# Kernel tuning notes

Hardware: AMD Instinct MI355X
Metric: run time of the kernel (lower is better)

## Reference

```python
import jax, jax.numpy as jnp
import numpy as np

NUM_USERS = 100000
NUM_ITEMS = 50000
EMB_DIM = 64
NUM_LAYERS = 3
NUM_EDGES = 1000000


def _xavier(key, shape):
    fan_in, fan_out = shape[-1], shape[-2] if len(shape) > 1 else shape[-1]
    limit = float(np.sqrt(6.0 / (fan_in + fan_out)))
    return jax.random.uniform(key, shape, jnp.float32, -limit, limit)


def setup_inputs() -> dict:
    key = jax.random.key(0)
    ks = jax.random.split(key, 8)
    edge_u = jax.random.randint(ks[0], (NUM_EDGES,), 0, NUM_USERS)
    edge_i = jax.random.randint(ks[1], (NUM_EDGES,), 0, NUM_ITEMS)
    u_emb = _xavier(ks[2], (NUM_USERS, EMB_DIM))
    i_emb = _xavier(ks[3], (NUM_ITEMS, EMB_DIM))
    Wgc = _xavier(ks[4], (NUM_LAYERS, EMB_DIM, EMB_DIM))
    Wbi = _xavier(ks[5], (NUM_LAYERS, EMB_DIM, EMB_DIM))
    bgc = jnp.zeros((NUM_LAYERS, EMB_DIM), jnp.float32)
    bbi = jnp.zeros((NUM_LAYERS, EMB_DIM), jnp.float32)
    return {"u_emb": u_emb, "i_emb": i_emb, "Wgc": Wgc, "bgc": bgc,
            "Wbi": Wbi, "bbi": bbi, "edge_u": edge_u, "edge_i": edge_i}


def _smooth(X, src, dst, dv_isqrt, de_inv, num_v, num_e):
    # HGNN smoothing: D_v^{-1/2} H D_e^{-1} H^T D_v^{-1/2} X via edge list
    X1 = X * dv_isqrt[:, None]
    E = jax.ops.segment_sum(X1[src], dst, num_segments=num_e) * de_inv[:, None]
    Y = jax.ops.segment_sum(E[dst], src, num_segments=num_v)
    return Y * dv_isqrt[:, None]


def reference(u_emb, i_emb, Wgc, bgc, Wbi, bbi, edge_u, edge_i):
    NU, NI, D = u_emb.shape[0], i_emb.shape[0], u_emb.shape[1]
    ones = jnp.ones((edge_u.shape[0],), jnp.float32)
    deg_u = jax.ops.segment_sum(ones, edge_u, num_segments=NU)
    deg_i = jax.ops.segment_sum(ones, edge_i, num_segments=NI)
    du_isqrt = jnp.where(deg_u > 0, deg_u, 1.0) ** -0.5 * (deg_u > 0)
    di_isqrt = jnp.where(deg_i > 0, deg_i, 1.0) ** -0.5 * (deg_i > 0)
    du_inv = jnp.where(deg_u > 0, 1.0 / jnp.where(deg_u > 0, deg_u, 1.0), 0.0)
    di_inv = jnp.where(deg_i > 0, 1.0 / jnp.where(deg_i > 0, deg_i, 1.0), 0.0)

    all_embs = jnp.concatenate([u_emb, i_emb], axis=0)
    embs_list = [all_embs]
    for l in range(Wgc.shape[0]):
        u, i = all_embs[:NU], all_embs[NU:]
        # hg_ui: users = vertices, items = hyperedges
        u_s = _smooth(u, edge_u, edge_i, du_isqrt, di_inv, NU, NI)
        # hg_iu: items = vertices, users = hyperedges
        i_s = _smooth(i, edge_i, edge_u, di_isqrt, du_inv, NI, NU)
        g = jnp.concatenate([u_s, i_s], axis=0)
        sum_embs = jax.nn.leaky_relu(g @ Wgc[l].T + bgc[l] + all_embs, negative_slope=0.2)
        bi_embs = jax.nn.leaky_relu((all_embs * g) @ Wbi[l].T + bbi[l], negative_slope=0.2)
        all_embs = sum_embs + bi_embs  # dropout off (eval mode)
        norm = jnp.sqrt(jnp.sum(all_embs * all_embs, axis=1, keepdims=True))
        all_embs = all_embs / jnp.maximum(norm, 1e-12)
        embs_list.append(all_embs)
    embs = jnp.mean(jnp.stack(embs_list, axis=1), axis=1)
    return embs[:NU], embs[NU:]
```

## Files before the change

### kernel.cpp

```cpp
#include <hip/hip_runtime.h>
#include <cstdint>
#include <cstddef>

#define NU 100000
#define NI 50000
#define NTOT 150000
#define EDIM 64
#define NE 1000000
#define NLAYERS 3
#define NTILES (NTOT / 16)
#define NPAIR (NTOT / 2)

#define NBKT 256
#define NPB 586
#define BCAP 13312
#define BCUR_STRIDE 16
#define BIN_EPB 1024
#define BIN_NBLK ((NE + BIN_EPB - 1) / BIN_EPB)
#define LCAP 28
#define LPAD 29
#define SLICE_CAP 13312

typedef __attribute__((ext_vector_type(8))) short short8;
typedef __attribute__((ext_vector_type(4))) float floatx4;

__device__ inline unsigned short f2bf(float f) {
    unsigned u = __float_as_uint(f);
    u += 0x7fffu + ((u >> 16) & 1u);
    return (unsigned short)(u >> 16);
}
__device__ inline unsigned pack_bf2(float a, float b) {
    unsigned ua = __float_as_uint(a); ua += 0x7fffu + ((ua >> 16) & 1u);
    unsigned ub = __float_as_uint(b); ub += 0x7fffu + ((ub >> 16) & 1u);
    return (ua >> 16) | (ub & 0xffff0000u);
}
__device__ inline float bf_lo(unsigned u) { return __uint_as_float(u << 16); }
__device__ inline float bf_hi(unsigned u) { return __uint_as_float(u & 0xffff0000u); }

__global__ __launch_bounds__(256) void k_binpairs(const int* __restrict__ eu,
                                                  const int* __restrict__ ei,
                                                  unsigned* __restrict__ bcur,
                                                  unsigned* __restrict__ bbuf) {
    __shared__ unsigned lbuf[NBKT * LPAD];
    __shared__ int lcnt[NBKT];
    int t = threadIdx.x;
    if (t < NBKT) lcnt[t] = 0;
    __syncthreads();
    int ebase = blockIdx.x * BIN_EPB + t;
#pragma unroll
    for (int k = 0; k < 4; ++k) {
        int e = ebase + k * 256;
        if (e < NE) {
            int u = eu[e];
            int v = NU + ei[e];
            int b0 = u / NPB;
            int w0 = ((u - b0 * NPB) << 18) | v;
            int p0 = atomicAdd(&lcnt[b0], 1);
            if (p0 < LCAP) lbuf[b0 * LPAD + p0] = (unsigned)w0;
            else {
                unsigned gp = atomicAdd(&bcur[b0 * BCUR_STRIDE], 1u);
                if (gp < BCAP) bbuf[(size_t)b0 * BCAP + gp] = (unsigned)w0;
            }
            int b1 = v / NPB;
            int w1 = ((v - b1 * NPB) << 18) | u;
            int p1 = atomicAdd(&lcnt[b1], 1);
            if (p1 < LCAP) lbuf[b1 * LPAD + p1] = (unsigned)w1;
            else {
                unsigned gp = atomicAdd(&bcur[b1 * BCUR_STRIDE], 1u);
                if (gp < BCAP) bbuf[(size_t)b1 * BCAP + gp] = (unsigned)w1;
            }
        }
    }
    __syncthreads();
    int nb = min(lcnt[t], LCAP);
    if (nb > 0) {
        unsigned gp = atomicAdd(&bcur[t * BCUR_STRIDE], (unsigned)nb);
        for (int i = 0; i < nb; ++i) {
            unsigned idx = gp + i;
            if (idx < BCAP) bbuf[(size_t)t * BCAP + idx] = lbuf[t * LPAD + i];
        }
    }
}

__global__ __launch_bounds__(1024) void k_buildcsr(
    const unsigned* __restrict__ bbuf, const unsigned* __restrict__ bcur,
    int* __restrict__ deg, int* __restrict__ start,
    float* __restrict__ isq, float* __restrict__ inv, int* __restrict__ csr,
    const float* __restrict__ ue, const float* __restrict__ ie,
    unsigned* __restrict__ snap0, unsigned* __restrict__ gbuf,
    unsigned* __restrict__ Ebuf,
    const float* __restrict__ Wg, const float* __restrict__ Wb,
    unsigned short* __restrict__ wgb, unsigned short* __restrict__ wbb) {
    __shared__ int slice[SLICE_CAP];
    __shared__ int lcur[NPB];
    __shared__ float sisq[NPB];
    __shared__ int bb_s, scnt_s;
    int b = blockIdx.x;
    int t = threadIdx.x;
    int n0 = b * NPB;
    int nn = NTOT - n0;
    if (nn > NPB) nn = NPB;
    if (nn < 0) nn = 0;
    if (t < NBKT) slice[t] = min((int)bcur[t * BCUR_STRIDE], BCAP);
    if (t < NPB) lcur[t] = 0;
    __syncthreads();
    for (int off = 1; off < NBKT; off <<= 1) {
        int tmp = (t < NBKT && t >= off) ? slice[t - off] : 0;
        __syncthreads();
        if (t < NBKT) slice[t] += tmp;
        __syncthreads();
    }
    if (t == 0) {
        int tb = min((int)bcur[b * BCUR_STRIDE], BCAP);
        scnt_s = tb;
        bb_s = slice[b] - tb;
    }
    __syncthreads();
    int c = scnt_s;
    int bb = bb_s;
    const unsigned* pb = bbuf + (size_t)b * BCAP;
    for (int i = t; i < c; i += 1024) atomicAdd(&lcur[(int)(pb[i] >> 18)], 1);
    __syncthreads();
    int cnt_t = (t < nn) ? lcur[t] : 0;
    slice[t] = cnt_t;
    __syncthreads();
    for (int off = 1; off < 1024; off <<= 1) {
        int tmp = (t >= off) ? slice[t - off] : 0;
        __syncthreads();
        slice[t] += tmp;
        __syncthreads();
    }
    int excl = slice[t] - cnt_t;
    int slen = slice[1023];
    if (t < nn) {
        int n = n0 + t;
        deg[n] = cnt_t;
        start[n] = bb + excl;
        float df = (float)cnt_t;
        float q = cnt_t > 0 ? 1.0f / sqrtf(df) : 0.f;
        isq[n] = q;
        sisq[t] = q;
        inv[n] = cnt_t > 0 ? 1.0f / df : 0.f;
    }
    __syncthreads();
    if (t < nn) lcur[t] = excl;
    __syncthreads();
    for (int i = t; i < c; i += 1024) {
        unsigned pr = pb[i];
        int idx = atomicAdd(&lcur[(int)(pr >> 18)], 1);
        if (idx < SLICE_CAP) slice[idx] = (int)(pr & 0x3FFFFu);
    }
    __syncthreads();
    if (slen > SLICE_CAP) slen = SLICE_CAP;
    for (int i = t; i < slen; i += 1024) csr[bb + i] = slice[i];
    for (int idx = t; idx < nn * 16; idx += 1024) {
        int r = idx >> 4, cc = idx & 15;
        int n = n0 + r;
        float4 v = (n < NU) ? ((const float4*)ue)[(size_t)n * 16 + cc]
                            : ((const float4*)ie)[(size_t)(n - NU) * 16 + cc];
        float s = sisq[r];
        uint2 bq, bs;
        bq.x = pack_bf2(v.x, v.y);
        bq.y = pack_bf2(v.z, v.w);
        bs.x = pack_bf2(v.x * s, v.y * s);
        bs.y = pack_bf2(v.z * s, v.w * s);
        ((uint2*)snap0)[(size_t)n * 16 + cc] = bq;
        ((uint2*)gbuf)[(size_t)n * 16 + cc] = bs;
    }
    if (b == 0) {
        for (int i = t; i < NLAYERS * 4096 / 4; i += 1024) {
            float4 g4 = ((const float4*)Wg)[i];
            float4 b4 = ((const float4*)Wb)[i];
            uint2 g, bq;
            g.x = pack_bf2(g4.x, g4.y); g.y = pack_bf2(g4.z, g4.w);
            bq.x = pack_bf2(b4.x, b4.y); bq.y = pack_bf2(b4.z, b4.w);
            ((uint2*)wgb)[i] = g;
            ((uint2*)wbb)[i] = bq;
        }
        if (t < 16) {
            ((uint2*)(Ebuf + NTOT * 32))[t] = make_uint2(0u, 0u);
            ((uint2*)(gbuf + NTOT * 32))[t] = make_uint2(0u, 0u);
        }
    }
}

__global__ __launch_bounds__(256) void k_gather(
    const unsigned* __restrict__ in_bf, unsigned* __restrict__ out_bf,
    const int* __restrict__ csr, const int* __restrict__ start,
    const int* __restrict__ deg, const float* __restrict__ sA) {
    int gw = (blockIdx.x * 256 + threadIdx.x) >> 6;
    int lane = threadIdx.x & 63;
    if (gw >= NPAIR) return;
    int l2 = lane & 31;
    int hbase = lane & 32;
    int row = gw * 2 + (lane >> 5);
    int s = l2 & 7;
    int g = l2 >> 3;
    int s0 = start[row];
    int dg = deg[row];
    float sc = sA[row];
    int dgo = __shfl_xor(dg, 32);
    int dgmax = max(dg, dgo);
    float aL0 = 0.f, aL1 = 0.f, aL2 = 0.f, aL3 = 0.f;
    float aH0 = 0.f, aH1 = 0.f, aH2 = 0.f, aH3 = 0.f;
    for (int j0 = 0; j0 < dgmax; j0 += 32) {
        int nidx = NTOT;
        if (j0 + l2 < dg) nidx = csr[s0 + j0 + l2];
        int jlim = min(32, dgmax - j0);
        for (int j = 0; j < jlim; j += 16) {
            int m0 = __shfl(nidx, hbase + j + g);
            int m1 = __shfl(nidx, hbase + j + 4 + g);
            int m2 = __shfl(nidx, hbase + j + 8 + g);
            int m3 = __shfl(nidx, hbase + j + 12 + g);
            uint4 u0 = *(const uint4*)(in_bf + (size_t)m0 * 32 + s * 4);
            uint4 u1 = *(const uint4*)(in_bf + (size_t)m1 * 32 + s * 4);
            uint4 u2 = *(const uint4*)(in_bf + (size_t)m2 * 32 + s * 4);
            uint4 u3 = *(const uint4*)(in_bf + (size_t)m3 * 32 + s * 4);
            aL0 += bf_lo(u0.x); aH0 += bf_hi(u0.x);
            aL1 += bf_lo(u0.y); aH1 += bf_hi(u0.y);
            aL2 += bf_lo(u0.z); aH2 += bf_hi(u0.z);
            aL3 += bf_lo(u0.w); aH3 += bf_hi(u0.w);
            aL0 += bf_lo(u1.x); aH0 += bf_hi(u1.x);
            aL1 += bf_lo(u1.y); aH1 += bf_hi(u1.y);
            aL2 += bf_lo(u1.z); aH2 += bf_hi(u1.z);
            aL3 += bf_lo(u1.w); aH3 += bf_hi(u1.w);
            aL0 += bf_lo(u2.x); aH0 += bf_hi(u2.x);
            aL1 += bf_lo(u2.y); aH1 += bf_hi(u2.y);
            aL2 += bf_lo(u2.z); aH2 += bf_hi(u2.z);
            aL3 += bf_lo(u2.w); aH3 += bf_hi(u2.w);
            aL0 += bf_lo(u3.x); aH0 += bf_hi(u3.x);
            aL1 += bf_lo(u3.y); aH1 += bf_hi(u3.y);
            aL2 += bf_lo(u3.z); aH2 += bf_hi(u3.z);
            aL3 += bf_lo(u3.w); aH3 += bf_hi(u3.w);
        }
    }
#pragma unroll
    for (int m = 8; m <= 16; m <<= 1) {
        aL0 += __shfl_xor(aL0, m); aH0 += __shfl_xor(aH0, m);
        aL1 += __shfl_xor(aL1, m); aH1 += __shfl_xor(aH1, m);
        aL2 += __shfl_xor(aL2, m); aH2 += __shfl_xor(aH2, m);
        aL3 += __shfl_xor(aL3, m); aH3 += __shfl_xor(aH3, m);
    }
    if (g == 0) {
        uint4 o;
        o.x = pack_bf2(sc * aL0, sc * aH0);
        o.y = pack_bf2(sc * aL1, sc * aH1);
        o.z = pack_bf2(sc * aL2, sc * aH2);
        o.w = pack_bf2(sc * aL3, sc * aH3);
        *(uint4*)(out_bf + (size_t)row * 32 + s * 4) = o;
    }
}

__global__ __launch_bounds__(256) void k_dense_mfma(
    const unsigned short* __restrict__ a_prev, unsigned* gbuf,
    unsigned short* __restrict__ snap_l, const float* __restrict__ isq,
    const unsigned short* __restrict__ wgb, const unsigned short* __restrict__ wbb,
    const float* __restrict__ bg, const float* __restrict__ bb, int writeScaled,
    int finalOut, const unsigned short* __restrict__ s1,
    const float* __restrict__ ue, const float* __restrict__ ie,
    float* __restrict__ outp) {
    int lane = threadIdx.x & 63;
    int lanelo = lane & 15;
    int quad = lane >> 4;
    int wid = (blockIdx.x * blockDim.x + threadIdx.x) >> 6;
    if (wid >= NTILES) return;

    short8 bWg[4][2], bWb[4][2];
#pragma unroll
    for (int t = 0; t < 4; ++t) {
#pragma unroll
        for (int h = 0; h < 2; ++h) {
            int n = t * 16 + lanelo;
            int k0 = h * 32 + quad * 8;
            bWg[t][h] = *(const short8*)&wgb[n * 64 + k0];
            bWb[t][h] = *(const short8*)&wbb[n * 64 + k0];
        }
    }
    float bgv[4], bbv[4];
#pragma unroll
    for (int t = 0; t < 4; ++t) {
        bgv[t] = bg[t * 16 + lanelo];
        bbv[t] = bb[t * 16 + lanelo];
    }

    int rbase = wid * 16;
    int arow = rbase + lanelo;
    short8 aG[2], aAG[2];
#pragma unroll
    for (int h = 0; h < 2; ++h) {
        uint4 ug = *(const uint4*)(gbuf + arow * 32 + h * 16 + quad * 4);
        uint4 ua = *(const uint4*)((const unsigned*)a_prev + arow * 32 + h * 16 + quad * 4);
        aG[h] = *(const short8*)&ug;
        uint4 up;
        up.x = pack_bf2(bf_lo(ua.x) * bf_lo(ug.x), bf_hi(ua.x) * bf_hi(ug.x));
        up.y = pack_bf2(bf_lo(ua.y) * bf_lo(ug.y), bf_hi(ua.y) * bf_hi(ug.y));
        up.z = pack_bf2(bf_lo(ua.z) * bf_lo(ug.z), bf_hi(ua.z) * bf_hi(ug.z));
        up.w = pack_bf2(bf_lo(ua.w) * bf_lo(ug.w), bf_hi(ua.w) * bf_hi(ug.w));
        aAG[h] = *(const short8*)&up;
    }
    floatx4 accg[4], accb[4];
#pragma unroll
    for (int t = 0; t < 4; ++t) {
        accg[t] = (floatx4)(0.f);
        accb[t] = (floatx4)(0.f);
    }
#pragma unroll
    for (int t = 0; t < 4; ++t) {
#pragma unroll
        for (int h = 0; h < 2; ++h) {
            accg[t] = __builtin_amdgcn_mfma_f32_16x16x32_bf16(aG[h], bWg[t][h], accg[t], 0, 0, 0);
            accb[t] = __builtin_amdgcn_mfma_f32_16x16x32_bf16(aAG[h], bWb[t][h], accb[t], 0, 0, 0);
        }
    }
    float nv[4][4];
    float ss[4] = {0.f, 0.f, 0.f, 0.f};
#pragma unroll
    for (int i = 0; i < 4; ++i) {
        int r = rbase + quad * 4 + i;
#pragma unroll
        for (int t = 0; t < 4; ++t) {
            float a = __uint_as_float((unsigned)a_prev[r * 64 + t * 16 + lanelo] << 16);
            float e1 = accg[t][i] + bgv[t] + a;
            e1 = e1 >= 0.f ? e1 : 0.2f * e1;
            float e2 = accb[t][i] + bbv[t];
            e2 = e2 >= 0.f ? e2 : 0.2f * e2;
            float v = e1 + e2;
            nv[i][t] = v;
            ss[i] += v * v;
        }
    }
#pragma unroll
    for (int m = 1; m < 16; m <<= 1) {
#pragma unroll
        for (int i = 0; i < 4; ++i) ss[i] += __shfl_xor(ss[i], m, 64);
    }
#pragma unroll
    for (int i = 0; i < 4; ++i) {
        int r = rbase + quad * 4 + i;
        float rn = 1.0f / fmaxf(sqrtf(ss[i]), 1e-12f);
        float sc = isq[r] * rn;
        if (finalOut) {
#pragma unroll
            for (int t = 0; t < 4; ++t) {
                int idx = r * 64 + t * 16 + lanelo;
                float rr = nv[i][t] * rn;
                float s1v = __uint_as_float((unsigned)s1[idx] << 16);
                float s2v = __uint_as_float((unsigned)a_prev[idx] << 16);
                float ev = (r < NU) ? ue[idx] : ie[idx - NU * 64];
                outp[idx] = 0.25f * (ev + s1v + s2v + rr);
            }
        } else {
#pragma unroll
            for (int t = 0; t < 4; ++t) {
                int idx = r * 64 + t * 16 + lanelo;
                float rr = nv[i][t] * rn;
                snap_l[idx] = f2bf(rr);
                if (writeScaled)
                    ((unsigned short*)gbuf)[idx] = f2bf(nv[i][t] * sc);
            }
        }
    }
}


extern "C" void kernel_launch(void* const* d_in, const int* in_sizes, int n_in,
                              void* d_out, int out_size, void* d_ws, size_t ws_size,
                              hipStream_t stream) {
    const float* u_emb = (const float*)d_in[0];
    const float* i_emb = (const float*)d_in[1];
    const float* Wgc = (const float*)d_in[2];
    const float* bgc = (const float*)d_in[3];
    const float* Wbi = (const float*)d_in[4];
    const float* bbi = (const float*)d_in[5];
    const int* edge_u = (const int*)d_in[6];
    const int* edge_i = (const int*)d_in[7];
    float* out = (float*)d_out;

    char* w = (char*)d_ws;
    auto alloc = [&](size_t bytes) {
        char* p = w;
        w += (bytes + 255) & ~(size_t)255;
        return p;
    };
    const size_t ROWBYTES = (size_t)(NTOT + 1) * EDIM * 2;
    int* deg = (int*)alloc((size_t)NTOT * 4);
    int* start = (int*)alloc((size_t)NTOT * 4);
    unsigned* bcur = (unsigned*)alloc((size_t)NBKT * BCUR_STRIDE * 4);
    int* csr = (int*)alloc((size_t)2 * NE * 4);
    float* isq = (float*)alloc((size_t)NTOT * 4);
    float* inv = (float*)alloc((size_t)NTOT * 4);
    unsigned short* wgb = (unsigned short*)alloc((size_t)NLAYERS * 4096 * 2);
    unsigned short* wbb = (unsigned short*)alloc((size_t)NLAYERS * 4096 * 2);
    unsigned* snap0 = (unsigned*)alloc((size_t)NTOT * EDIM * 2);
    unsigned* snap1 = (unsigned*)alloc((size_t)NTOT * EDIM * 2);
    unsigned* snap2 = (unsigned*)alloc((size_t)NTOT * EDIM * 2);
    unsigned* Ebuf = (unsigned*)alloc(ROWBYTES);
    unsigned* gbuf = (unsigned*)alloc(ROWBYTES);
    unsigned* bbuf = (unsigned*)snap1;

    hipMemsetAsync(bcur, 0, (size_t)NBKT * BCUR_STRIDE * 4, stream);
    k_binpairs<<<BIN_NBLK, 256, 0, stream>>>(edge_u, edge_i, bcur, bbuf);
    k_buildcsr<<<NBKT, 1024, 0, stream>>>(bbuf, bcur, deg, start, isq, inv, csr,
                                          u_emb, i_emb, snap0, gbuf, Ebuf,
                                          Wgc, Wbi, wgb, wbb);

    const int gatherBlocks = (NPAIR * 64 + 255) / 256;
    const int denseBlocks = (NTILES * 64 + 255) / 256;
    const unsigned short* aprev[3] = {(unsigned short*)snap0, (unsigned short*)snap1,
                                      (unsigned short*)snap2};
    unsigned short* snaps[3] = {(unsigned short*)snap1, (unsigned short*)snap2,
                                (unsigned short*)snap1 };
    for (int l = 0; l < NLAYERS; ++l) {
        k_gather<<<gatherBlocks, 256, 0, stream>>>(gbuf, Ebuf, csr, start, deg, inv);
        k_gather<<<gatherBlocks, 256, 0, stream>>>(Ebuf, gbuf, csr, start, deg, isq);
        k_dense_mfma<<<denseBlocks, 256, 0, stream>>>(
            aprev[l], gbuf, snaps[l], isq, wgb + (size_t)l * 4096, wbb + (size_t)l * 4096,
            bgc + (size_t)l * 64, bbi + (size_t)l * 64,
            l < NLAYERS - 1 ? 1 : 0,
            l == NLAYERS - 1 ? 1 : 0,
            (const unsigned short*)snap1, u_emb, i_emb, out);
    }
}
```

Measured before the change: 456.5 us.

## Pair gather rows by degree via per-block permutation and add 4-wide tail loop

While building the CSR, each block sorts its rows into a permutation by degree bucket (capped at 63), and the gather kernel processes rows in that order. Two rows that share a wavefront then have similar degrees, so less time is lost when one half waits on the other's longer neighbour list. The inner loop also gains a 4-neighbour remainder step, so leftover neighbours no longer run a full 16-wide iteration of padded loads. The cost is an extra perm array read per row and the loss of row-order locality in the gather output writes.

```diff
diff --git a/kernel.cpp b/kernel.cpp
--- a/kernel.cpp
+++ b/kernel.cpp
@@ -90,7 +90,8 @@
     unsigned* __restrict__ snap0, unsigned* __restrict__ gbuf,
     unsigned* __restrict__ Ebuf,
     const float* __restrict__ Wg, const float* __restrict__ Wb,
-    unsigned short* __restrict__ wgb, unsigned short* __restrict__ wbb) {
+    unsigned short* __restrict__ wgb, unsigned short* __restrict__ wbb,
+    int* __restrict__ perm) {
     __shared__ int slice[SLICE_CAP];
     __shared__ int lcur[NPB];
     __shared__ float sisq[NPB];
@@ -153,6 +154,21 @@
     __syncthreads();
     if (slen > SLICE_CAP) slen = SLICE_CAP;
     for (int i = t; i < slen; i += 1024) csr[bb + i] = slice[i];
+    __syncthreads();
+    if (t < 64) lcur[t] = 0;
+    __syncthreads();
+    int mybin = -1, myrank = 0;
+    if (t < nn) {
+        mybin = cnt_t < 63 ? cnt_t : 63;
+        myrank = atomicAdd(&lcur[mybin], 1);
+    }
+    __syncthreads();
+    if (t == 0) {
+        int s = 0;
+        for (int q = 0; q < 64; ++q) { int cc = lcur[q]; lcur[q] = s; s += cc; }
+    }
+    __syncthreads();
+    if (t < nn) perm[n0 + lcur[mybin] + myrank] = n0 + t;
     for (int idx = t; idx < nn * 16; idx += 1024) {
         int r = idx >> 4, cc = idx & 15;
         int n = n0 + r;
@@ -187,13 +203,14 @@
 __global__ __launch_bounds__(256) void k_gather(
     const unsigned* __restrict__ in_bf, unsigned* __restrict__ out_bf,
     const int* __restrict__ csr, const int* __restrict__ start,
-    const int* __restrict__ deg, const float* __restrict__ sA) {
+    const int* __restrict__ deg, const float* __restrict__ sA,
+    const int* __restrict__ perm) {
     int gw = (blockIdx.x * 256 + threadIdx.x) >> 6;
     int lane = threadIdx.x & 63;
     if (gw >= NPAIR) return;
     int l2 = lane & 31;
     int hbase = lane & 32;
-    int row = gw * 2 + (lane >> 5);
+    int row = perm[gw * 2 + (lane >> 5)];
     int s = l2 & 7;
     int g = l2 >> 3;
     int s0 = start[row];
@@ -207,7 +224,8 @@
         int nidx = NTOT;
         if (j0 + l2 < dg) nidx = csr[s0 + j0 + l2];
         int jlim = min(32, dgmax - j0);
-        for (int j = 0; j < jlim; j += 16) {
+        int j = 0;
+        for (; j + 16 <= jlim; j += 16) {
             int m0 = __shfl(nidx, hbase + j + g);
             int m1 = __shfl(nidx, hbase + j + 4 + g);
             int m2 = __shfl(nidx, hbase + j + 8 + g);
@@ -233,6 +251,14 @@
             aL2 += bf_lo(u3.z); aH2 += bf_hi(u3.z);
             aL3 += bf_lo(u3.w); aH3 += bf_hi(u3.w);
         }
+        for (; j < jlim; j += 4) {
+            int m0 = __shfl(nidx, hbase + j + g);
+            uint4 u0 = *(const uint4*)(in_bf + (size_t)m0 * 32 + s * 4);
+            aL0 += bf_lo(u0.x); aH0 += bf_hi(u0.x);
+            aL1 += bf_lo(u0.y); aH1 += bf_hi(u0.y);
+            aL2 += bf_lo(u0.z); aH2 += bf_hi(u0.z);
+            aL3 += bf_lo(u0.w); aH3 += bf_hi(u0.w);
+        }
     }
 #pragma unroll
     for (int m = 8; m <= 16; m <<= 1) {
@@ -385,6 +411,7 @@
     const size_t ROWBYTES = (size_t)(NTOT + 1) * EDIM * 2;
     int* deg = (int*)alloc((size_t)NTOT * 4);
     int* start = (int*)alloc((size_t)NTOT * 4);
+    int* perm = (int*)alloc((size_t)NTOT * 4);
     unsigned* bcur = (unsigned*)alloc((size_t)NBKT * BCUR_STRIDE * 4);
     int* csr = (int*)alloc((size_t)2 * NE * 4);
     float* isq = (float*)alloc((size_t)NTOT * 4);
@@ -402,7 +429,7 @@
     k_binpairs<<<BIN_NBLK, 256, 0, stream>>>(edge_u, edge_i, bcur, bbuf);
     k_buildcsr<<<NBKT, 1024, 0, stream>>>(bbuf, bcur, deg, start, isq, inv, csr,
                                           u_emb, i_emb, snap0, gbuf, Ebuf,
-                                          Wgc, Wbi, wgb, wbb);
+                                          Wgc, Wbi, wgb, wbb, perm);
 
     const int gatherBlocks = (NPAIR * 64 + 255) / 256;
     const int denseBlocks = (NTILES * 64 + 255) / 256;
@@ -411,8 +438,8 @@
     unsigned short* snaps[3] = {(unsigned short*)snap1, (unsigned short*)snap2,
                                 (unsigned short*)snap1 };
     for (int l = 0; l < NLAYERS; ++l) {
-        k_gather<<<gatherBlocks, 256, 0, stream>>>(gbuf, Ebuf, csr, start, deg, inv);
-        k_gather<<<gatherBlocks, 256, 0, stream>>>(Ebuf, gbuf, csr, start, deg, isq);
+        k_gather<<<gatherBlocks, 256, 0, stream>>>(gbuf, Ebuf, csr, start, deg, inv, perm);
+        k_gather<<<gatherBlocks, 256, 0, stream>>>(Ebuf, gbuf, csr, start, deg, isq, perm);
         k_dense_mfma<<<denseBlocks, 256, 0, stream>>>(
             aprev[l], gbuf, snaps[l], isq, wgb + (size_t)l * 4096, wbb + (size_t)l * 4096,
             bgc + (size_t)l * 64, bbi + (size_t)l * 64,
```

Result: slower. 494.1 us (+8.2%).
